# Kernel tuning notes

Measured on AMD Instinct MI355X. Metric: run time of the kernel, lower is better.

## Reference

```python
import jax, jax.numpy as jnp
import numpy as np

D = 20   # max displacement (pad)
K = 21   # window side: 41x41 neighborhood sampled with stride 2 -> 21x21 = 441 offsets


def setup_inputs() -> dict:
    key = jax.random.key(0)
    k1, k2 = jax.random.split(key)
    features_1 = jax.random.normal(k1, (1, 256, 48, 64), dtype=jnp.float32)
    features_2 = jax.random.normal(k2, (1, 256, 48, 64), dtype=jnp.float32)
    return {"features_1": features_1, "features_2": features_2}


def _correlation(f1, f2):
    # f1, f2: [1, C, H, W]; torch code squeezes batch (batch must be 1)
    f1 = f1[0]
    f2 = f2[0]
    C, H, W = f1.shape  # (256, 48, 64)
    padded = jnp.pad(f2, ((0, 0), (D, D), (D, D)))  # [C, H+2D, W+2D]

    offs = 2 * jnp.arange(K, dtype=jnp.int32)  # stride-2 sampling of the 41x41 window
    oy, ox = jnp.meshgrid(offs, offs, indexing="ij")  # row-major flatten matches torch .flatten()
    offsets = jnp.stack([oy.reshape(-1), ox.reshape(-1)], axis=1)  # [441, 2]

    def corr_at(o):
        # shifted view of padded f2 for this displacement: [C, H, W]
        win = jax.lax.dynamic_slice(padded, (jnp.int32(0), o[0], o[1]), (C, H, W))
        return jnp.sum(f1 * win, axis=0)  # [H, W], dot over channels

    result = jax.vmap(corr_at)(offsets)  # [441, H, W]
    return result[None]  # [1, 441, H, W]


def reference(features_1, features_2):
    return _correlation(features_1, features_2)
```

## Files before the change

kernel.cpp:

```cpp
#include <hip/hip_runtime.h>

#define H 48
#define W 64
#define C 256
#define NK 21
#define HW (H * W)
#define LDS_STRIDE 528
#define LDS_TENSOR (64 * LDS_STRIDE)

typedef __attribute__((ext_vector_type(8))) short bf16x8;
typedef __attribute__((ext_vector_type(4))) float f32x4;

__device__ __forceinline__ unsigned pack2bf(float a, float b) {
  unsigned ua = __builtin_bit_cast(unsigned, a);
  unsigned ub = __builtin_bit_cast(unsigned, b);
  ua = (ua + 0x7FFFu + ((ua >> 16) & 1u)) >> 16;
  ub = (ub + 0x7FFFu + ((ub >> 16) & 1u)) & 0xFFFF0000u;
  return ua | ub;
}

__device__ __forceinline__ void stage_row(const float* __restrict__ src, char* lds, int tid) {
  const int lane = tid & 63, wave = tid >> 6;
  const float* col = src + lane;
#pragma unroll
  for (int i = 0; i < 8; ++i) {
    const int oct = i * 4 + wave;
    const float* p = col + (size_t)oct * 8 * HW;
    float v0 = p[0], v1 = p[HW], v2 = p[2 * HW], v3 = p[3 * HW];
    float v4 = p[4 * HW], v5 = p[5 * HW], v6 = p[6 * HW], v7 = p[7 * HW];
    uint4 w;
    w.x = pack2bf(v0, v1);
    w.y = pack2bf(v2, v3);
    w.z = pack2bf(v4, v5);
    w.w = pack2bf(v6, v7);
    *reinterpret_cast<uint4*>(lds + lane * LDS_STRIDE + oct * 16) = w;
  }
}

__global__ __launch_bounds__(256, 2) void corr_fused(
    const float* __restrict__ f1, const float* __restrict__ f2, float* __restrict__ out) {
  __shared__ char smem[2 * LDS_TENSOR];
  const int b = blockIdx.x;
  const int y = b / NK, oyi = b % NK;
  const int r = y + 2 * oyi - 20;
  const int tid = threadIdx.x;
  float* outBase = out + (size_t)(oyi * NK) * HW + y * W;

  if ((unsigned)r >= (unsigned)H) {
    for (int i = tid; i < NK * W; i += 256) {
      int oxi = i >> 6, x = i & 63;
      outBase[(size_t)oxi * HW + x] = 0.f;
    }
    return;
  }

  stage_row(f1 + (size_t)y * W, smem, tid);
  stage_row(f2 + (size_t)r * W, smem + LDS_TENSOR, tid);
  __syncthreads();

  const int wave = tid >> 6, lane = tid & 63;
  f32x4 acc[4] = {};
  const int koff = (lane >> 4) * 16;
  const char* aRow = smem + (wave * 16 + (lane & 15)) * LDS_STRIDE + koff;
  const char* bBase = smem + LDS_TENSOR + (lane & 15) * LDS_STRIDE + koff;
#pragma unroll
  for (int ks = 0; ks < 8; ++ks) {
    bf16x8 a = *reinterpret_cast<const bf16x8*>(aRow + ks * 64);
#pragma unroll
    for (int tn = 0; tn < 4; ++tn) {
      bf16x8 bb = *reinterpret_cast<const bf16x8*>(bBase + tn * 16 * LDS_STRIDE + ks * 64);
      acc[tn] = __builtin_amdgcn_mfma_f32_16x16x32_bf16(a, bb, acc[tn], 0, 0, 0);
    }
  }
  __syncthreads();

  float* M = (float*)smem;
#pragma unroll
  for (int tn = 0; tn < 4; ++tn) {
#pragma unroll
    for (int j = 0; j < 4; ++j) {
      int x1 = (wave << 4) + ((lane >> 4) << 2) + j;
      int x2 = (tn << 4) + (lane & 15);
      M[x1 * 66 + x2] = acc[tn][j];
    }
  }
  __syncthreads();

  for (int i = tid; i < NK * W; i += 256) {
    int oxi = i >> 6, x = i & 63;
    int x2 = x + 2 * oxi - 20;
    float v = ((unsigned)x2 < (unsigned)W) ? M[x * 66 + x2] : 0.f;
    outBase[(size_t)oxi * HW + x] = v;
  }
}

extern "C" void kernel_launch(void* const* d_in, const int* in_sizes, int n_in,
                              void* d_out, int out_size, void* d_ws, size_t ws_size,
                              hipStream_t stream) {
  (void)in_sizes; (void)n_in; (void)d_ws; (void)ws_size; (void)out_size;
  const float* f1 = (const float*)d_in[0];
  const float* f2 = (const float*)d_in[1];
  float* out = (float*)d_out;
  corr_fused<<<H * NK, 256, 0, stream>>>(f1, f2, out);
}
```

Measured before the change: 18.89 us.

## Pair vertical offsets per block to reuse staged f1 row, split K in halves

Each block now handles two vertical displacement rows, so the f1 row is staged once and reused for both correlations. This halves the block count and the redundant f1 loads and bf16 conversions. The channel dimension is staged in two halves so three tensors fit in less LDS, and launch bounds are raised to 3 blocks per CU. The cost is an extra sync round, more serial work per block, and possible imbalance, since the last group has only one row.

New measurement: 19.57 us. 1.04x slower.

```diff
diff --git a/kernel.cpp b/kernel.cpp
--- a/kernel.cpp
+++ b/kernel.cpp
@@ -5,8 +5,9 @@
 #define C 256
 #define NK 21
 #define HW (H * W)
-#define LDS_STRIDE 528
-#define LDS_TENSOR (64 * LDS_STRIDE)
+#define NG 11
+#define HSTRIDE 272
+#define HTENSOR (64 * HSTRIDE)
 
 typedef __attribute__((ext_vector_type(8))) short bf16x8;
 typedef __attribute__((ext_vector_type(4))) float f32x4;
@@ -19,11 +20,12 @@
   return ua | ub;
 }
 
-__device__ __forceinline__ void stage_row(const float* __restrict__ src, char* lds, int tid) {
+__device__ __forceinline__ void stage_half(const float* __restrict__ src, char* lds,
+                                           int kh, int tid) {
   const int lane = tid & 63, wave = tid >> 6;
-  const float* col = src + lane;
+  const float* col = src + (size_t)kh * 128 * HW + lane;
 #pragma unroll
-  for (int i = 0; i < 8; ++i) {
+  for (int i = 0; i < 4; ++i) {
     const int oct = i * 4 + wave;
     const float* p = col + (size_t)oct * 8 * HW;
     float v0 = p[0], v1 = p[HW], v2 = p[2 * HW], v3 = p[3 * HW];
@@ -33,64 +35,108 @@
     w.y = pack2bf(v2, v3);
     w.z = pack2bf(v4, v5);
     w.w = pack2bf(v6, v7);
-    *reinterpret_cast<uint4*>(lds + lane * LDS_STRIDE + oct * 16) = w;
+    *reinterpret_cast<uint4*>(lds + lane * HSTRIDE + oct * 16) = w;
   }
 }
 
-__global__ __launch_bounds__(256, 2) void corr_fused(
+__global__ __launch_bounds__(256, 3) void corr_pair(
     const float* __restrict__ f1, const float* __restrict__ f2, float* __restrict__ out) {
-  __shared__ char smem[2 * LDS_TENSOR];
+  __shared__ char smem[3 * HTENSOR];
   const int b = blockIdx.x;
-  const int y = b / NK, oyi = b % NK;
-  const int r = y + 2 * oyi - 20;
+  const int y = b / NG, g = b % NG;
+  const int oy0 = 2 * g, oy1 = 2 * g + 1;
+  const bool ex1 = (oy1 < NK);
+  const int r0 = y + 2 * oy0 - 20;
+  const int r1 = y + 2 * oy1 - 20;
+  const bool v0 = (unsigned)r0 < (unsigned)H;
+  const bool v1 = ex1 && ((unsigned)r1 < (unsigned)H);
   const int tid = threadIdx.x;
-  float* outBase = out + (size_t)(oyi * NK) * HW + y * W;
+  const int wave = tid >> 6, lane = tid & 63;
 
-  if ((unsigned)r >= (unsigned)H) {
+  auto zerofill = [&](int oyi) {
+    float* ob = out + (size_t)(oyi * NK) * HW + y * W;
     for (int i = tid; i < NK * W; i += 256) {
       int oxi = i >> 6, x = i & 63;
-      outBase[(size_t)oxi * HW + x] = 0.f;
+      ob[(size_t)oxi * HW + x] = 0.f;
     }
+  };
+
+  if (!v0 && !v1) {
+    zerofill(oy0);
+    if (ex1) zerofill(oy1);
     return;
   }
 
-  stage_row(f1 + (size_t)y * W, smem, tid);
-  stage_row(f2 + (size_t)r * W, smem + LDS_TENSOR, tid);
-  __syncthreads();
+  f32x4 acc0[4] = {};
+  f32x4 acc1[4] = {};
 
-  const int wave = tid >> 6, lane = tid & 63;
-  f32x4 acc[4] = {};
-  const int koff = (lane >> 4) * 16;
-  const char* aRow = smem + (wave * 16 + (lane & 15)) * LDS_STRIDE + koff;
-  const char* bBase = smem + LDS_TENSOR + (lane & 15) * LDS_STRIDE + koff;
 #pragma unroll
-  for (int ks = 0; ks < 8; ++ks) {
-    bf16x8 a = *reinterpret_cast<const bf16x8*>(aRow + ks * 64);
+  for (int kh = 0; kh < 2; ++kh) {
+    if (kh) __syncthreads();
+    stage_half(f1 + (size_t)y * W, smem, kh, tid);
+    if (v0) stage_half(f2 + (size_t)r0 * W, smem + HTENSOR, kh, tid);
+    if (v1) stage_half(f2 + (size_t)r1 * W, smem + 2 * HTENSOR, kh, tid);
+    __syncthreads();
+
+    const int koff = (lane >> 4) << 4;
+    const char* aRow = smem + (wave * 16 + (lane & 15)) * HSTRIDE + koff;
+    if (v0) {
+      const char* bRow = smem + HTENSOR + (lane & 15) * HSTRIDE + koff;
 #pragma unroll
-    for (int tn = 0; tn < 4; ++tn) {
-      bf16x8 bb = *reinterpret_cast<const bf16x8*>(bBase + tn * 16 * LDS_STRIDE + ks * 64);
-      acc[tn] = __builtin_amdgcn_mfma_f32_16x16x32_bf16(a, bb, acc[tn], 0, 0, 0);
+      for (int ks = 0; ks < 4; ++ks) {
+        bf16x8 a = *reinterpret_cast<const bf16x8*>(aRow + ks * 64);
+#pragma unroll
+        for (int tn = 0; tn < 4; ++tn) {
+          bf16x8 bb = *reinterpret_cast<const bf16x8*>(bRow + (tn * 16) * HSTRIDE + ks * 64);
+          acc0[tn] = __builtin_amdgcn_mfma_f32_16x16x32_bf16(a, bb, acc0[tn], 0, 0, 0);
+        }
+      }
+    }
+    if (v1) {
+      const char* bRow = smem + 2 * HTENSOR + (lane & 15) * HSTRIDE + koff;
+#pragma unroll
+      for (int ks = 0; ks < 4; ++ks) {
+        bf16x8 a = *reinterpret_cast<const bf16x8*>(aRow + ks * 64);
+#pragma unroll
+        for (int tn = 0; tn < 4; ++tn) {
+          bf16x8 bb = *reinterpret_cast<const bf16x8*>(bRow + (tn * 16) * HSTRIDE + ks * 64);
+          acc1[tn] = __builtin_amdgcn_mfma_f32_16x16x32_bf16(a, bb, acc1[tn], 0, 0, 0);
+        }
+      }
     }
   }
   __syncthreads();
 
   float* M = (float*)smem;
+
+  auto emit = [&](const f32x4* acc, int oyi) {
+    float* ob = out + (size_t)(oyi * NK) * HW + y * W;
 #pragma unroll
-  for (int tn = 0; tn < 4; ++tn) {
+    for (int tn = 0; tn < 4; ++tn) {
 #pragma unroll
-    for (int j = 0; j < 4; ++j) {
-      int x1 = (wave << 4) + ((lane >> 4) << 2) + j;
-      int x2 = (tn << 4) + (lane & 15);
-      M[x1 * 66 + x2] = acc[tn][j];
+      for (int j = 0; j < 4; ++j) {
+        int x1 = (wave << 4) + ((lane >> 4) << 2) + j;
+        int x2 = (tn << 4) + (lane & 15);
+        M[x1 * 66 + x2] = acc[tn][j];
+      }
     }
-  }
-  __syncthreads();
+    __syncthreads();
+    for (int i = tid; i < NK * W; i += 256) {
+      int oxi = i >> 6, x = i & 63;
+      int x2 = x + 2 * oxi - 20;
+      float v = ((unsigned)x2 < (unsigned)W) ? M[x * 66 + x2] : 0.f;
+      ob[(size_t)oxi * HW + x] = v;
+    }
+  };
 
-  for (int i = tid; i < NK * W; i += 256) {
-    int oxi = i >> 6, x = i & 63;
-    int x2 = x + 2 * oxi - 20;
-    float v = ((unsigned)x2 < (unsigned)W) ? M[x * 66 + x2] : 0.f;
-    outBase[(size_t)oxi * HW + x] = v;
+  if (v0) emit(acc0, oy0); else zerofill(oy0);
+  if (ex1) {
+    if (v1) {
+      __syncthreads();
+      emit(acc1, oy1);
+    } else {
+      zerofill(oy1);
+    }
   }
 }
 
@@ -101,5 +147,5 @@
   const float* f1 = (const float*)d_in[0];
   const float* f2 = (const float*)d_in[1];
   float* out = (float*)d_out;
-  corr_fused<<<H * NK, 256, 0, stream>>>(f1, f2, out);
+  corr_pair<<<H * NG, 256, 0, stream>>>(f1, f2, out);
 }
```

## Stage channels in two halves to halve LDS and raise occupancy

Applied to the files above, without the earlier changes.

Splits the 256-channel reduction into two 128-channel phases. Each phase stages a half-sized bf16 tile of both rows into LDS and runs its MFMAs before the next half is loaded, which halves shared memory per block and lets launch bounds ask for 4 blocks per CU instead of 2. The bf16 packing also switches from manual bit arithmetic to the HIP intrinsic. In exchange it adds an extra barrier and serialises load and compute between the halves.

Measured after the change: 16.83 us. 10.9% less time.

```diff
diff --git a/kernel.cpp b/kernel.cpp
--- a/kernel.cpp
+++ b/kernel.cpp
@@ -1,29 +1,30 @@
 #include <hip/hip_runtime.h>
+#include <hip/hip_bf16.h>
 
 #define H 48
 #define W 64
 #define C 256
 #define NK 21
 #define HW (H * W)
-#define LDS_STRIDE 528
-#define LDS_TENSOR (64 * LDS_STRIDE)
+#define HSTRIDE 272
+#define HTENSOR (64 * HSTRIDE)
 
 typedef __attribute__((ext_vector_type(8))) short bf16x8;
 typedef __attribute__((ext_vector_type(4))) float f32x4;
 
 __device__ __forceinline__ unsigned pack2bf(float a, float b) {
-  unsigned ua = __builtin_bit_cast(unsigned, a);
-  unsigned ub = __builtin_bit_cast(unsigned, b);
-  ua = (ua + 0x7FFFu + ((ua >> 16) & 1u)) >> 16;
-  ub = (ub + 0x7FFFu + ((ub >> 16) & 1u)) & 0xFFFF0000u;
-  return ua | ub;
+  __hip_bfloat162 h = __float22bfloat162_rn(make_float2(a, b));
+  unsigned u;
+  __builtin_memcpy(&u, &h, 4);
+  return u;
 }
 
-__device__ __forceinline__ void stage_row(const float* __restrict__ src, char* lds, int tid) {
+__device__ __forceinline__ void stage_half(const float* __restrict__ src, char* lds,
+                                           int kh, int tid) {
   const int lane = tid & 63, wave = tid >> 6;
-  const float* col = src + lane;
+  const float* col = src + (size_t)kh * 128 * HW + lane;
 #pragma unroll
-  for (int i = 0; i < 8; ++i) {
+  for (int i = 0; i < 4; ++i) {
     const int oct = i * 4 + wave;
     const float* p = col + (size_t)oct * 8 * HW;
     float v0 = p[0], v1 = p[HW], v2 = p[2 * HW], v3 = p[3 * HW];
@@ -33,13 +34,13 @@
     w.y = pack2bf(v2, v3);
     w.z = pack2bf(v4, v5);
     w.w = pack2bf(v6, v7);
-    *reinterpret_cast<uint4*>(lds + lane * LDS_STRIDE + oct * 16) = w;
+    *reinterpret_cast<uint4*>(lds + lane * HSTRIDE + oct * 16) = w;
   }
 }
 
-__global__ __launch_bounds__(256, 2) void corr_fused(
+__global__ __launch_bounds__(256, 4) void corr_fused(
     const float* __restrict__ f1, const float* __restrict__ f2, float* __restrict__ out) {
-  __shared__ char smem[2 * LDS_TENSOR];
+  __shared__ char smem[2 * HTENSOR];
   const int b = blockIdx.x;
   const int y = b / NK, oyi = b % NK;
   const int r = y + 2 * oyi - 20;
@@ -54,22 +55,27 @@
     return;
   }
 
-  stage_row(f1 + (size_t)y * W, smem, tid);
-  stage_row(f2 + (size_t)r * W, smem + LDS_TENSOR, tid);
-  __syncthreads();
-
   const int wave = tid >> 6, lane = tid & 63;
   f32x4 acc[4] = {};
-  const int koff = (lane >> 4) * 16;
-  const char* aRow = smem + (wave * 16 + (lane & 15)) * LDS_STRIDE + koff;
-  const char* bBase = smem + LDS_TENSOR + (lane & 15) * LDS_STRIDE + koff;
+  const int koff = (lane >> 4) << 4;
+
 #pragma unroll
-  for (int ks = 0; ks < 8; ++ks) {
-    bf16x8 a = *reinterpret_cast<const bf16x8*>(aRow + ks * 64);
+  for (int kh = 0; kh < 2; ++kh) {
+    if (kh) __syncthreads();
+    stage_half(f1 + (size_t)y * W, smem, kh, tid);
+    stage_half(f2 + (size_t)r * W, smem + HTENSOR, kh, tid);
+    __syncthreads();
+
+    const char* aRow = smem + (wave * 16 + (lane & 15)) * HSTRIDE + koff;
+    const char* bRow = smem + HTENSOR + (lane & 15) * HSTRIDE + koff;
 #pragma unroll
-    for (int tn = 0; tn < 4; ++tn) {
-      bf16x8 bb = *reinterpret_cast<const bf16x8*>(bBase + tn * 16 * LDS_STRIDE + ks * 64);
-      acc[tn] = __builtin_amdgcn_mfma_f32_16x16x32_bf16(a, bb, acc[tn], 0, 0, 0);
+    for (int ks = 0; ks < 4; ++ks) {
+      bf16x8 a = *reinterpret_cast<const bf16x8*>(aRow + ks * 64);
+#pragma unroll
+      for (int tn = 0; tn < 4; ++tn) {
+        bf16x8 bb = *reinterpret_cast<const bf16x8*>(bRow + (tn * 16) * HSTRIDE + ks * 64);
+        acc[tn] = __builtin_amdgcn_mfma_f32_16x16x32_bf16(a, bb, acc[tn], 0, 0, 0);
+      }
     }
   }
   __syncthreads();
```
